# Kernel optimization log

Measured on AMD Instinct MI355X. Metric: run time of the kernel, lower is better.

Reference implementation:

```python
import jax, jax.numpy as jnp
import numpy as np

B, S, DIM = 2, 2048, 2048
NH, NKV = 32, 8
HD = DIM // NH          # 64
NREP = NH // NKV        # 4
BASE = 10000.0


def setup_inputs() -> dict:
    key = jax.random.key(0)
    ks = jax.random.split(key, 5)
    x = jax.random.normal(ks[0], (B, S, DIM), dtype=jnp.float32)
    # causal mask, 1 = keep, 0 = masked (matches masked_fill(mask == 0, -inf))
    mask = jnp.tril(jnp.ones((S, S), dtype=jnp.float32))[None, None]
    scale = 0.02
    Wq = jax.random.normal(ks[1], (DIM, NH * HD), dtype=jnp.float32) * scale
    Wk = jax.random.normal(ks[2], (DIM, NKV * HD), dtype=jnp.float32) * scale
    Wv = jax.random.normal(ks[3], (DIM, NKV * HD), dtype=jnp.float32) * scale
    Wo = jax.random.normal(ks[4], (NH * HD, DIM), dtype=jnp.float32) * scale
    return {"x": x, "mask": mask, "Wq": Wq, "Wk": Wk, "Wv": Wv, "Wo": Wo}


def _rope_cos_sin(seq_len, head_dim, dtype):
    inv_freq = 1.0 / (BASE ** (jnp.arange(0, head_dim, 2, dtype=jnp.float32) / head_dim))
    t = jnp.arange(seq_len, dtype=jnp.float32)
    freqs = t[:, None] * inv_freq[None, :]            # [S, HD/2]
    return jnp.cos(freqs).astype(dtype), jnp.sin(freqs).astype(dtype)


def _apply_rope(x, cos, sin):
    # x: [B, H, S, HD]; cos/sin: [S, HD/2] broadcast over B,H
    x1, x2 = jnp.split(x, 2, axis=-1)
    c = cos[None, None]
    s = sin[None, None]
    return jnp.concatenate([x1 * c - x2 * s, x2 * c + x1 * s], axis=-1)


def reference(x, mask, Wq, Wk, Wv, Wo):
    b, s, _ = x.shape
    q = (x @ Wq).reshape(b, s, NH, HD).transpose(0, 2, 1, 3)   # [B,NH,S,HD]
    k = (x @ Wk).reshape(b, s, NKV, HD).transpose(0, 2, 1, 3)  # [B,NKV,S,HD]
    v = (x @ Wv).reshape(b, s, NKV, HD).transpose(0, 2, 1, 3)
    cos, sin = _rope_cos_sin(s, HD, x.dtype)
    q = _apply_rope(q, cos, sin)
    k = _apply_rope(k, cos, sin)
    # GQA: repeat kv heads
    k = jnp.repeat(k, NREP, axis=1)
    v = jnp.repeat(v, NREP, axis=1)
    scale = HD ** -0.5
    attn = jnp.einsum('bhqd,bhkd->bhqk', q, k) * scale
    attn = jnp.where(mask == 0, -jnp.inf, attn)
    attn = jax.nn.softmax(attn, axis=-1)
    out = jnp.einsum('bhqk,bhkd->bhqd', attn, v)
    out = out.transpose(0, 2, 1, 3).reshape(b, s, NH * HD)
    return out @ Wo
```

## Files before the change

### kernel.cpp

```cpp
#include <hip/hip_runtime.h>
#include <stdint.h>

typedef __attribute__((ext_vector_type(8))) short short8;
typedef __attribute__((ext_vector_type(4))) short short4v;
typedef __attribute__((ext_vector_type(4))) float float4v;
typedef __attribute__((ext_vector_type(16))) float f32x16;
typedef __attribute__((ext_vector_type(4))) int int4v;
typedef __attribute__((ext_vector_type(2))) int int2v;
typedef __attribute__((ext_vector_type(2))) unsigned int uint2v;

#define DEV __device__ __forceinline__

DEV ushort f2bf(float f){
  uint32_t u = __float_as_uint(f);
  u = (u + 0x7fffu + ((u >> 16) & 1u)) >> 16;
  return (ushort)u;
}
DEV float bf2f(ushort h){
  uint32_t u = ((uint32_t)h) << 16;
  return __uint_as_float(u);
}

DEV void gload16(const void* g, void* l){
  __builtin_amdgcn_global_load_lds((const __attribute__((address_space(1))) void*)g,
                                   (__attribute__((address_space(3))) void*)l, 16, 0, 0);
}

DEV uint32_t cvtpk(float lo, float hi){
  uint32_t d;
  asm("v_cvt_pk_bf16_f32 %0, %1, %2" : "=v"(d) : "v"(lo), "v"(hi));
  return d;
}

DEV uint2v plswap2(uint32_t a, uint32_t b){
  return __builtin_amdgcn_permlane32_swap(a, b, false, false);
}

__global__ __launch_bounds__(256) void k_prep(const float* __restrict__ x, const float* __restrict__ Wq,
                                              const float* __restrict__ Wk, const float* __restrict__ Wv,
                                              const float* __restrict__ Wo,
                                              ushort* __restrict__ xb, ushort* __restrict__ wqkvt,
                                              ushort* __restrict__ wot,
                                              float* __restrict__ cost, float* __restrict__ sint,
                                              float qscale){
  __shared__ float tile[32][33];
  const int bid = blockIdx.x;
  if (bid < 10240){
    const float* src; ushort* dst; int N, K, bx, by; float scale;
    if (bid < 4096){ src = Wq; dst = wqkvt; N = 2048; K = 2048; scale = qscale; bx = bid & 63; by = bid >> 6; }
    else if (bid < 5120){ int lb = bid - 4096; src = Wk; dst = wqkvt + (size_t)2048 * 2048; N = 512; K = 2048; scale = 1.f; bx = lb & 15; by = lb >> 4; }
    else if (bid < 6144){ int lb = bid - 5120; src = Wv; dst = wqkvt + (size_t)2560 * 2048; N = 512; K = 2048; scale = 1.f; bx = lb & 15; by = lb >> 4; }
    else { int lb = bid - 6144; src = Wo; dst = wot; N = 2048; K = 2048; scale = 1.f; bx = lb & 63; by = lb >> 6; }
    int c0 = bx * 32, r0 = by * 32;
    int tx = threadIdx.x & 31, ty = threadIdx.x >> 5;
    #pragma unroll
    for (int i = 0; i < 32; i += 8)
      tile[ty + i][tx] = src[(size_t)(r0 + ty + i) * N + (c0 + tx)];
    __syncthreads();
    #pragma unroll
    for (int i = 0; i < 32; i += 8)
      dst[(size_t)(c0 + ty + i) * K + (r0 + tx)] = f2bf(tile[tx][ty + i] * scale);
  } else if (bid < 10496){
    int i = (bid - 10240) * 256 + threadIdx.x;
    int s = i >> 5, d = i & 31;
    float inv = powf(10000.0f, -(float)d / 32.0f);
    float ang = (float)s * inv;
    float sv, cv;
    sincosf(ang, &sv, &cv);
    cost[i] = cv;
    sint[i] = sv;
  } else {
    int i = (bid - 10496) * 256 + threadIdx.x;
    float4v v = *(const float4v*)(x + (size_t)i * 4);
    short4v o;
    o[0] = (short)f2bf(v[0]); o[1] = (short)f2bf(v[1]);
    o[2] = (short)f2bf(v[2]); o[3] = (short)f2bf(v[3]);
    *(short4v*)(xb + (size_t)i * 4) = o;
  }
}

template<int BM, int BN, bool OUTF32, int MINW>
__global__ __launch_bounds__(512, MINW) void k_gemm8(const ushort* __restrict__ A, const ushort* __restrict__ Bt,
                                                     void* __restrict__ Cp, int M, int N, int K, int nbx){
  constexpr int WM = BM / 2, WN = BN / 4;
  constexpr int MR = WM / 16, NR = WN / 16, MP = MR / 4;
  constexpr int AISS = BM / 64, BISS = BN / 64;
  constexpr int BUFB = (BM + BN) * 128;
  __shared__ char lds[2 * BUFB];

  int wg = blockIdx.x;
  int cpx = (int)gridDim.x >> 3;
  wg = (wg & 7) * cpx + (wg >> 3);
  const int bn = wg % nbx, bm = wg / nbx;
  const int tid = threadIdx.x;
  const int w = tid >> 6, l = tid & 63, l15 = l & 15, hi = l >> 4;
  const int wr = w >> 2, wc = w & 3;

  const int r8 = tid >> 3;
  const int ce = ((tid & 7) ^ (r8 & 7)) << 3;
  const ushort* ag = A + (size_t)(bm * BM + r8) * K + ce;
  const ushort* bg = Bt + (size_t)(bn * BN + r8) * K + ce;

  float4v acc[MR][NR];
  #pragma unroll
  for (int a = 0; a < MR; ++a)
    #pragma unroll
    for (int b = 0; b < NR; ++b)
      acc[a][b] = (float4v){0.f, 0.f, 0.f, 0.f};

  auto stage = [&](int kt, int buf){
    char* ab = lds + buf * BUFB;
    char* bb = ab + BM * 128;
    #pragma unroll
    for (int i = 0; i < AISS; ++i)
      gload16(ag + (size_t)(i * 64) * K + kt * 64, ab + i * 8192 + tid * 16);
    #pragma unroll
    for (int i = 0; i < BISS; ++i)
      gload16(bg + (size_t)(i * 64) * K + kt * 64, bb + i * 8192 + tid * 16);
  };
  auto lda = [&](const char* ab, int mf, int kk)->short8{
    int row = wr * WM + mf * 16 + l15;
    int a = (row * 128 + kk * 64 + hi * 16) ^ ((row & 7) << 4);
    return *(const short8*)(ab + a);
  };
  auto ldb = [&](const char* bb, int nf, int kk)->short8{
    int row = wc * WN + nf * 16 + l15;
    int a = (row * 128 + kk * 64 + hi * 16) ^ ((row & 7) << 4);
    return *(const short8*)(bb + a);
  };

  const int nkt = K >> 6;
  stage(0, 0);
  for (int t = 0; t < nkt; ++t){
    asm volatile("s_waitcnt vmcnt(0)" ::: "memory");
    __builtin_amdgcn_s_barrier();
    __builtin_amdgcn_sched_barrier(0);
    if (t + 1 < nkt) stage(t + 1, (t + 1) & 1);

    const char* ab = lds + (t & 1) * BUFB;
    const char* bb = ab + BM * 128;
    short8 bfr[NR][2];
    #pragma unroll
    for (int nf = 0; nf < NR; ++nf){ bfr[nf][0] = ldb(bb, nf, 0); bfr[nf][1] = ldb(bb, nf, 1); }
    short8 af[MP][2];
    #pragma unroll
    for (int ml = 0; ml < MP; ++ml){ af[ml][0] = lda(ab, ml, 0); af[ml][1] = lda(ab, ml, 1); }

    #pragma unroll
    for (int p = 0; p < 4; ++p){
      asm volatile("s_waitcnt lgkmcnt(0)" ::: "memory");
      __builtin_amdgcn_sched_barrier(0);
      __builtin_amdgcn_s_setprio(1);
      #pragma unroll
      for (int ml = 0; ml < MP; ++ml)
        #pragma unroll
        for (int nf = 0; nf < NR; ++nf){
          const int mf = p * MP + ml;
          acc[mf][nf] = __builtin_amdgcn_mfma_f32_16x16x32_bf16(af[ml][0], bfr[nf][0], acc[mf][nf], 0, 0, 0);
          acc[mf][nf] = __builtin_amdgcn_mfma_f32_16x16x32_bf16(af[ml][1], bfr[nf][1], acc[mf][nf], 0, 0, 0);
        }
      __builtin_amdgcn_s_setprio(0);
      __builtin_amdgcn_sched_barrier(0);
      if (p < 3){
        #pragma unroll
        for (int ml = 0; ml < MP; ++ml){
          af[ml][0] = lda(ab, (p + 1) * MP + ml, 0);
          af[ml][1] = lda(ab, (p + 1) * MP + ml, 1);
        }
      }
    }
  }

  #pragma unroll
  for (int mf = 0; mf < MR; ++mf){
    int row0 = bm * BM + wr * WM + mf * 16 + hi * 4;
    #pragma unroll
    for (int nf = 0; nf < NR; ++nf){
      int col = bn * BN + wc * WN + nf * 16 + l15;
      #pragma unroll
      for (int reg = 0; reg < 4; ++reg){
        size_t idx = (size_t)(row0 + reg) * N + col;
        if constexpr (OUTF32) ((float*)Cp)[idx] = acc[mf][nf][reg];
        else                  ((ushort*)Cp)[idx] = f2bf(acc[mf][nf][reg]);
      }
    }
  }
}

__global__ __launch_bounds__(256) void k_rope_vt(ushort* __restrict__ qkv, const float* __restrict__ cost,
                                                 const float* __restrict__ sint, ushort* __restrict__ vt){
  __shared__ ushort tile[64][72];
  const int bid = blockIdx.x;
  if (bid < 5120){
    int t = bid * 256 + threadIdx.x;
    int row = t / 320;
    int rem = t - row * 320;
    int head = rem >> 3, d0 = (rem & 7) * 4;
    int s = row & 2047;
    ushort* p = qkv + (size_t)row * 3072 + head * 64 + d0;
    short4v a = *(short4v*)p;
    short4v b = *(short4v*)(p + 32);
    float4v c  = *(const float4v*)(cost + s * 32 + d0);
    float4v sn = *(const float4v*)(sint + s * 32 + d0);
    short4v na, nb;
    #pragma unroll
    for (int j = 0; j < 4; ++j){
      float x1 = bf2f((ushort)a[j]), x2 = bf2f((ushort)b[j]);
      na[j] = (short)f2bf(x1 * c[j] - x2 * sn[j]);
      nb[j] = (short)f2bf(x2 * c[j] + x1 * sn[j]);
    }
    *(short4v*)p = na;
    *(short4v*)(p + 32) = nb;
  } else {
    int lb = bid - 5120;
    int g = lb >> 5, st = lb & 31;
    int b = g >> 3, hk = g & 7;
    const ushort* src = qkv + (size_t)(b * 2048 + st * 64) * 3072 + 2560 + hk * 64;
    int tid = threadIdx.x;
    #pragma unroll
    for (int i = 0; i < 2; ++i){
      int r = i * 32 + (tid >> 3), c8 = (tid & 7) * 8;
      short8 v = *(const short8*)(src + (size_t)r * 3072 + c8);
      #pragma unroll
      for (int j = 0; j < 8; ++j) tile[r][c8 + j] = (ushort)v[j];
    }
    __syncthreads();
    ushort* dst = vt + (size_t)g * 64 * 2048 + st * 64;
    #pragma unroll
    for (int i = 0; i < 2; ++i){
      int d = i * 32 + (tid >> 3), s8 = (tid & 7) * 8;
      short8 ov;
      #pragma unroll
      for (int j = 0; j < 8; ++j) ov[j] = (short)tile[s8 + j][d];
      *(short8*)(dst + (size_t)d * 2048 + s8) = ov;
    }
  }
}

__global__ __launch_bounds__(256) void k_attn9(const ushort* __restrict__ qkv, const ushort* __restrict__ vt,
                                               ushort* __restrict__ att,
                                               ushort* __restrict__ pO, float* __restrict__ pl){
  __shared__ __align__(16) char lds[2][16384];
  const int id = blockIdx.x;
  int gidx, hloc, qb, t0, t1, slot = 0;
  bool split;
  if (id < 1024){
    int xcd = id & 7, s2 = id >> 3;
    gidx = xcd * 2 + (s2 >> 6);
    int idx6 = s2 & 63;
    hloc = idx6 & 3;
    int c = (idx6 >> 2) & 1;
    qb = 15 - (idx6 >> 3);
    int nt = 2 * qb + 2, hh = nt >> 1;
    t0 = c * hh; t1 = t0 + hh;
    split = true;
    slot = (((gidx * 4 + hloc) * 8) + (15 - qb)) * 2 + c;
  } else {
    int id2 = id - 1024;
    int xcd = id2 & 7, s3 = id2 >> 3;
    gidx = xcd * 2 + (s3 & 1);
    int idx5 = s3 >> 1;
    hloc = idx5 & 3;
    qb = 7 - (idx5 >> 2);
    t0 = 0; t1 = 2 * qb + 2;
    split = false;
  }
  const int b = gidx >> 3, hk = gidx & 7;
  const int h = hk * 4 + hloc;
  const int tid = threadIdx.x;
  const int w = tid >> 6, l = tid & 63, ql = l & 31, g = l >> 5;
  const int qw = qb * 128 + w * 32;
  const int diag_t = (qw + 31) >> 6;
  const int swz = (ql & 7) << 4;

  short8 qf[4];
  {
    const ushort* qbase = qkv + (size_t)(b * 2048 + qw + ql) * 3072 + h * 64 + g * 8;
    #pragma unroll
    for (int ds = 0; ds < 4; ++ds) qf[ds] = *(const short8*)(qbase + ds * 16);
  }
  short8 onesf;
  #pragma unroll
  for (int i = 0; i < 8; ++i) onesf[i] = (short)0x3F80;

  f32x16 o0, o1, ladd;
  #pragma unroll
  for (int r = 0; r < 16; ++r){ o0[r] = 0.f; o1[r] = 0.f; ladd[r] = 0.f; }

  const int srow = tid >> 3;
  const int ce = ((tid & 7) ^ (srow & 7)) << 3;
  const ushort* kg = qkv + (size_t)(b * 2048 + srow) * 3072 + 2048 + hk * 64 + ce;
  const ushort* vg = vt + (size_t)gidx * 64 * 2048 + (size_t)srow * 2048 + ce;

  auto stage = [&](int t, int buf){
    char* lb = lds[buf];
    #pragma unroll
    for (int i = 0; i < 2; ++i)
      gload16(kg + (size_t)(t * 64 + i * 32) * 3072, lb + i * 4096 + tid * 16);
    #pragma unroll
    for (int i = 0; i < 2; ++i)
      gload16(vg + (size_t)(i * 32) * 2048 + t * 64, lb + 8192 + i * 4096 + tid * 16);
  };

  stage(t0, t0 & 1);
  for (int t = t0; t < t1; ++t){
    asm volatile("s_waitcnt vmcnt(0)" ::: "memory");
    __builtin_amdgcn_s_barrier();
    __builtin_amdgcn_sched_barrier(0);
    if (t + 1 < t1) stage(t + 1, (t + 1) & 1);

    if (t <= diag_t){
      const char* Kb = lds[t & 1];
      const char* Vb = Kb + 8192;

      f32x16 sa0, sa1;
      #pragma unroll
      for (int r = 0; r < 16; ++r){ sa0[r] = 0.f; sa1[r] = 0.f; }
      __builtin_amdgcn_s_setprio(1);
      #pragma unroll
      for (int ds = 0; ds < 4; ++ds){
        int cb = (ds * 32 + g * 16) ^ swz;
        short8 k0 = *(const short8*)(Kb + ql * 128 + cb);
        short8 k1 = *(const short8*)(Kb + (32 + ql) * 128 + cb);
        sa0 = __builtin_amdgcn_mfma_f32_32x32x16_bf16(k0, qf[ds], sa0, 0, 0, 0);
        sa1 = __builtin_amdgcn_mfma_f32_32x32x16_bf16(k1, qf[ds], sa1, 0, 0, 0);
      }
      __builtin_amdgcn_s_setprio(0);

      if (t == diag_t){
        int thr = qw + ql - t * 64;
        #pragma unroll
        for (int r = 0; r < 16; ++r){
          int kl = (r & 3) + 8 * (r >> 2) + 4 * g;
          sa0[r] = (kl > thr) ? -3e38f : sa0[r];
          sa1[r] = (kl + 32 > thr) ? -3e38f : sa1[r];
        }
      }

      uint32_t wds[2][8];
      #pragma unroll
      for (int u = 0; u < 8; ++u){
        float a0 = __builtin_amdgcn_exp2f(sa0[2 * u]);
        float a1 = __builtin_amdgcn_exp2f(sa0[2 * u + 1]);
        wds[0][u] = cvtpk(a0, a1);
        float b0 = __builtin_amdgcn_exp2f(sa1[2 * u]);
        float b1 = __builtin_amdgcn_exp2f(sa1[2 * u + 1]);
        wds[1][u] = cvtpk(b0, b1);
      }

      __builtin_amdgcn_s_setprio(1);
      #pragma unroll
      for (int ks = 0; ks < 4; ++ks){
        const int s2 = ks >> 1, c4 = (ks & 1) * 4;
        uint2v e0 = plswap2(wds[s2][c4 + 0], wds[s2][c4 + 2]);
        uint2v e1 = plswap2(wds[s2][c4 + 1], wds[s2][c4 + 3]);
        union { int4v w4; short8 s8; } pb;
        pb.w4[0] = (int)e0[0]; pb.w4[1] = (int)e1[0];
        pb.w4[2] = (int)e0[1]; pb.w4[3] = (int)e1[1];
        int cb = (ks * 32 + g * 16) ^ swz;
        short8 v0 = *(const short8*)(Vb + ql * 128 + cb);
        short8 v1 = *(const short8*)(Vb + (32 + ql) * 128 + cb);
        o0 = __builtin_amdgcn_mfma_f32_32x32x16_bf16(v0, pb.s8, o0, 0, 0, 0);
        o1 = __builtin_amdgcn_mfma_f32_32x32x16_bf16(v1, pb.s8, o1, 0, 0, 0);
        ladd = __builtin_amdgcn_mfma_f32_32x32x16_bf16(onesf, pb.s8, ladd, 0, 0, 0);
      }
      __builtin_amdgcn_s_setprio(0);
    }
  }

  if (split){
    ushort* po = pO + (size_t)slot * 8192 + (size_t)(w * 32 + ql) * 64;
    #pragma unroll
    for (int dm = 0; dm < 2; ++dm){
      #pragma unroll
      for (int rg = 0; rg < 4; ++rg){
        float f0 = dm ? o1[4 * rg + 0] : o0[4 * rg + 0];
        float f1 = dm ? o1[4 * rg + 1] : o0[4 * rg + 1];
        float f2 = dm ? o1[4 * rg + 2] : o0[4 * rg + 2];
        float f3 = dm ? o1[4 * rg + 3] : o0[4 * rg + 3];
        int2v wv;
        wv[0] = (int)cvtpk(f0, f1);
        wv[1] = (int)cvtpk(f2, f3);
        *(int2v*)(po + dm * 32 + 8 * rg + 4 * g) = wv;
      }
    }
    if (!g) pl[slot * 128 + w * 32 + ql] = ladd[0];
  } else {
    float invl = 1.0f / ladd[0];
    ushort* ob = att + (size_t)(b * 2048 + qw + ql) * 2048 + h * 64;
    #pragma unroll
    for (int dm = 0; dm < 2; ++dm){
      #pragma unroll
      for (int rg = 0; rg < 4; ++rg){
        float f0 = (dm ? o1[4 * rg + 0] : o0[4 * rg + 0]) * invl;
        float f1 = (dm ? o1[4 * rg + 1] : o0[4 * rg + 1]) * invl;
        float f2 = (dm ? o1[4 * rg + 2] : o0[4 * rg + 2]) * invl;
        float f3 = (dm ? o1[4 * rg + 3] : o0[4 * rg + 3]) * invl;
        int2v wv;
        wv[0] = (int)cvtpk(f0, f1);
        wv[1] = (int)cvtpk(f2, f3);
        *(int2v*)(ob + dm * 32 + 8 * rg + 4 * g) = wv;
      }
    }
  }
}

__global__ __launch_bounds__(256) void k_combine(const ushort* __restrict__ pO, const float* __restrict__ pl,
                                                 ushort* __restrict__ att){
  const int id = blockIdx.x;
  const int pid = id >> 1, half = id & 1;
  const int head = pid >> 3, qb8 = pid & 7;
  const int qb = 15 - qb8;
  const int gidx = head >> 2, hloc = head & 3;
  const int b = gidx >> 3, hk = gidx & 7;
  const int h = hk * 4 + hloc;
  const int s0 = (head * 8 + qb8) * 2;
  const int tid = threadIdx.x;
  const int r = half * 64 + (tid >> 2);
  const int cc = (tid & 3) * 16;
  const ushort* A = pO + (size_t)s0 * 8192 + (size_t)r * 64 + cc;
  const ushort* B = A + 8192;
  float lsum = pl[s0 * 128 + r] + pl[(s0 + 1) * 128 + r];
  float inv = 1.0f / lsum;
  short8 xa0 = *(const short8*)A, xa1 = *(const short8*)(A + 8);
  short8 xb0 = *(const short8*)B, xb1 = *(const short8*)(B + 8);
  ushort* dst = att + (size_t)(b * 2048 + qb * 128 + r) * 2048 + h * 64 + cc;
  int4v w0, w1;
  #pragma unroll
  for (int j = 0; j < 4; ++j){
    float e0 = (bf2f((ushort)xa0[2 * j]) + bf2f((ushort)xb0[2 * j])) * inv;
    float e1 = (bf2f((ushort)xa0[2 * j + 1]) + bf2f((ushort)xb0[2 * j + 1])) * inv;
    w0[j] = (int)cvtpk(e0, e1);
    float e2 = (bf2f((ushort)xa1[2 * j]) + bf2f((ushort)xb1[2 * j])) * inv;
    float e3 = (bf2f((ushort)xa1[2 * j + 1]) + bf2f((ushort)xb1[2 * j + 1])) * inv;
    w1[j] = (int)cvtpk(e2, e3);
  }
  *(int4v*)dst = w0;
  *(int4v*)(dst + 8) = w1;
}

extern "C" void kernel_launch(void* const* d_in, const int* in_sizes, int n_in,
                              void* d_out, int out_size, void* d_ws, size_t ws_size,
                              hipStream_t stream) {
  const float* x  = (const float*)d_in[0];
  const float* Wq = (const float*)d_in[2];
  const float* Wk = (const float*)d_in[3];
  const float* Wv = (const float*)d_in[4];
  const float* Wo = (const float*)d_in[5];

  char* ws = (char*)d_ws;
  ushort* xb    = (ushort*)(ws);
  ushort* wqkvt = (ushort*)(ws + (16u << 20));
  ushort* wot   = (ushort*)(ws + (28u << 20));
  ushort* qkv   = (ushort*)(ws + (36u << 20));
  ushort* att   = (ushort*)(ws + (60u << 20));
  ushort* vt    = (ushort*)(ws + (76u << 20));
  float*  cost  = (float*)(ws + (80u << 20));
  float*  sint  = (float*)(ws + (80u << 20) + 262144);

  ushort* pO = xb;
  float*  pl = (float*)wqkvt;

  const float qscale = 0.125f * 1.4426950408889634f;

  k_prep<<<18688, 256, 0, stream>>>(x, Wq, Wk, Wv, Wo, xb, wqkvt, wot, cost, sint, qscale);
  k_gemm8<128, 192, false, 4><<<512, 512, 0, stream>>>(xb, wqkvt, qkv, 4096, 3072, 2048, 16);
  k_rope_vt<<<5632, 256, 0, stream>>>(qkv, cost, sint, vt);
  k_attn9<<<1536, 256, 0, stream>>>(qkv, vt, att, pO, pl);
  k_combine<<<1024, 256, 0, stream>>>(pO, pl, att);
  k_gemm8<128, 128, true, 4><<<512, 512, 0, stream>>>(att, wot, d_out, 4096, 2048, 2048, 16);
}
```

Measured before the change: 176.7 us.

## Rebalance causal attention work by pairing short and long query blocks per workgroup

Replaces the previous scheme (long query blocks split in two halves, short blocks one per workgroup) with a table-driven schedule. Each workgroup either processes a pair of complementary query blocks (qb and 7-qb) in sequence, or one half of a long block's key range. This cuts the launch from 1536 to 1280 workgroups with roughly equal work each, which should reduce tail imbalance. It also adds an occupancy hint of 5 in the launch bounds. The combine kernel's slot indexing is updated to match. The trade-offs are serial segments inside one workgroup and a possible register cap from the launch-bounds hint.

```diff
diff --git a/kernel.cpp b/kernel.cpp
--- a/kernel.cpp
+++ b/kernel.cpp
@@ -237,55 +237,29 @@
   }
 }
 
-__global__ __launch_bounds__(256) void k_attn9(const ushort* __restrict__ qkv, const ushort* __restrict__ vt,
-                                               ushort* __restrict__ att,
-                                               ushort* __restrict__ pO, float* __restrict__ pl){
+__global__ __launch_bounds__(256, 5) void k_attn11(const ushort* __restrict__ qkv, const ushort* __restrict__ vt,
+                                                   ushort* __restrict__ att,
+                                                   ushort* __restrict__ pO, float* __restrict__ pl){
+  static const signed char IT_Q[20] = {7,15,8,14, 6,15,8,14, 5,13,9,12, 4,13,9,12, 10,11,10,11};
+  static const signed char IT_H[20] = {-1,0,0,0, -1,1,1,1, -1,0,0,0, -1,1,1,1, 0,0,1,1};
   __shared__ __align__(16) char lds[2][16384];
   const int id = blockIdx.x;
-  int gidx, hloc, qb, t0, t1, slot = 0;
-  bool split;
-  if (id < 1024){
-    int xcd = id & 7, s2 = id >> 3;
-    gidx = xcd * 2 + (s2 >> 6);
-    int idx6 = s2 & 63;
-    hloc = idx6 & 3;
-    int c = (idx6 >> 2) & 1;
-    qb = 15 - (idx6 >> 3);
-    int nt = 2 * qb + 2, hh = nt >> 1;
-    t0 = c * hh; t1 = t0 + hh;
-    split = true;
-    slot = (((gidx * 4 + hloc) * 8) + (15 - qb)) * 2 + c;
-  } else {
-    int id2 = id - 1024;
-    int xcd = id2 & 7, s3 = id2 >> 3;
-    gidx = xcd * 2 + (s3 & 1);
-    int idx5 = s3 >> 1;
-    hloc = idx5 & 3;
-    qb = 7 - (idx5 >> 2);
-    t0 = 0; t1 = 2 * qb + 2;
-    split = false;
-  }
+  const int xcd = id & 7, lid = id >> 3;
+  const int gh = lid / 80, li = lid - gh * 80;
+  const int gidx = xcd * 2 + gh;
   const int b = gidx >> 3, hk = gidx & 7;
+  const int hloc = li / 20, it = li - hloc * 20;
   const int h = hk * 4 + hloc;
+  const int qb0 = IT_Q[it];
+  const int hh = IT_H[it];
+  const int nseg = (hh < 0) ? 2 : 1;
   const int tid = threadIdx.x;
   const int w = tid >> 6, l = tid & 63, ql = l & 31, g = l >> 5;
-  const int qw = qb * 128 + w * 32;
-  const int diag_t = (qw + 31) >> 6;
   const int swz = (ql & 7) << 4;
 
-  short8 qf[4];
-  {
-    const ushort* qbase = qkv + (size_t)(b * 2048 + qw + ql) * 3072 + h * 64 + g * 8;
-    #pragma unroll
-    for (int ds = 0; ds < 4; ++ds) qf[ds] = *(const short8*)(qbase + ds * 16);
-  }
   short8 onesf;
   #pragma unroll
   for (int i = 0; i < 8; ++i) onesf[i] = (short)0x3F80;
-
-  f32x16 o0, o1, ladd;
-  #pragma unroll
-  for (int r = 0; r < 16; ++r){ o0[r] = 0.f; o1[r] = 0.f; ladd[r] = 0.f; }
 
   const int srow = tid >> 3;
   const int ce = ((tid & 7) ^ (srow & 7)) << 3;
@@ -302,104 +276,126 @@
       gload16(vg + (size_t)(i * 32) * 2048 + t * 64, lb + 8192 + i * 4096 + tid * 16);
   };
 
-  stage(t0, t0 & 1);
-  for (int t = t0; t < t1; ++t){
-    asm volatile("s_waitcnt vmcnt(0)" ::: "memory");
-    __builtin_amdgcn_s_barrier();
-    __builtin_amdgcn_sched_barrier(0);
-    if (t + 1 < t1) stage(t + 1, (t + 1) & 1);
-
-    if (t <= diag_t){
-      const char* Kb = lds[t & 1];
-      const char* Vb = Kb + 8192;
-
-      f32x16 sa0, sa1;
-      #pragma unroll
-      for (int r = 0; r < 16; ++r){ sa0[r] = 0.f; sa1[r] = 0.f; }
-      __builtin_amdgcn_s_setprio(1);
-      #pragma unroll
-      for (int ds = 0; ds < 4; ++ds){
-        int cb = (ds * 32 + g * 16) ^ swz;
-        short8 k0 = *(const short8*)(Kb + ql * 128 + cb);
-        short8 k1 = *(const short8*)(Kb + (32 + ql) * 128 + cb);
-        sa0 = __builtin_amdgcn_mfma_f32_32x32x16_bf16(k0, qf[ds], sa0, 0, 0, 0);
-        sa1 = __builtin_amdgcn_mfma_f32_32x32x16_bf16(k1, qf[ds], sa1, 0, 0, 0);
+  for (int seg = 0; seg < nseg; ++seg){
+    const int qb = (hh < 0) ? (seg ? (7 - qb0) : qb0) : qb0;
+    int t0, t1;
+    bool partial;
+    if (hh < 0){ t0 = 0; t1 = 2 * qb + 2; partial = false; }
+    else { t0 = hh ? (qb0 + 1) : 0; t1 = hh ? (2 * qb0 + 2) : (qb0 + 1); partial = true; }
+    const int qw = qb * 128 + w * 32;
+    const int diag_t = (qw + 31) >> 6;
+
+    short8 qf[4];
+    {
+      const ushort* qbase = qkv + (size_t)(b * 2048 + qw + ql) * 3072 + h * 64 + g * 8;
+      #pragma unroll
+      for (int ds = 0; ds < 4; ++ds) qf[ds] = *(const short8*)(qbase + ds * 16);
+    }
+
+    f32x16 o0, o1, ladd;
+    #pragma unroll
+    for (int r = 0; r < 16; ++r){ o0[r] = 0.f; o1[r] = 0.f; ladd[r] = 0.f; }
+
+    stage(t0, t0 & 1);
+    for (int t = t0; t < t1; ++t){
+      asm volatile("s_waitcnt vmcnt(0)" ::: "memory");
+      __builtin_amdgcn_s_barrier();
+      __builtin_amdgcn_sched_barrier(0);
+      if (t + 1 < t1) stage(t + 1, (t + 1) & 1);
+
+      if (t <= diag_t){
+        const char* Kb = lds[t & 1];
+        const char* Vb = Kb + 8192;
+
+        f32x16 sa0, sa1;
+        #pragma unroll
+        for (int r = 0; r < 16; ++r){ sa0[r] = 0.f; sa1[r] = 0.f; }
+        __builtin_amdgcn_s_setprio(1);
+        #pragma unroll
+        for (int ds = 0; ds < 4; ++ds){
+          int cb = (ds * 32 + g * 16) ^ swz;
+          short8 k0 = *(const short8*)(Kb + ql * 128 + cb);
+          short8 k1 = *(const short8*)(Kb + (32 + ql) * 128 + cb);
+          sa0 = __builtin_amdgcn_mfma_f32_32x32x16_bf16(k0, qf[ds], sa0, 0, 0, 0);
+          sa1 = __builtin_amdgcn_mfma_f32_32x32x16_bf16(k1, qf[ds], sa1, 0, 0, 0);
+        }
+        __builtin_amdgcn_s_setprio(0);
+
+        if (t == diag_t){
+          int thr = qw + ql - t * 64;
+          #pragma unroll
+          for (int r = 0; r < 16; ++r){
+            int kl = (r & 3) + 8 * (r >> 2) + 4 * g;
+            sa0[r] = (kl > thr) ? -3e38f : sa0[r];
+            sa1[r] = (kl + 32 > thr) ? -3e38f : sa1[r];
+          }
+        }
+
+        uint32_t wds[2][8];
+        #pragma unroll
+        for (int u = 0; u < 8; ++u){
+          float a0 = __builtin_amdgcn_exp2f(sa0[2 * u]);
+          float a1 = __builtin_amdgcn_exp2f(sa0[2 * u + 1]);
+          wds[0][u] = cvtpk(a0, a1);
+          float b0 = __builtin_amdgcn_exp2f(sa1[2 * u]);
+          float b1 = __builtin_amdgcn_exp2f(sa1[2 * u + 1]);
+          wds[1][u] = cvtpk(b0, b1);
+        }
+
+        __builtin_amdgcn_s_setprio(1);
+        #pragma unroll
+        for (int ks = 0; ks < 4; ++ks){
+          const int s2 = ks >> 1, c4 = (ks & 1) * 4;
+          uint2v e0 = plswap2(wds[s2][c4 + 0], wds[s2][c4 + 2]);
+          uint2v e1 = plswap2(wds[s2][c4 + 1], wds[s2][c4 + 3]);
+          union { int4v w4; short8 s8; } pb;
+          pb.w4[0] = (int)e0[0]; pb.w4[1] = (int)e1[0];
+          pb.w4[2] = (int)e0[1]; pb.w4[3] = (int)e1[1];
+          int cb = (ks * 32 + g * 16) ^ swz;
+          short8 v0 = *(const short8*)(Vb + ql * 128 + cb);
+          short8 v1 = *(const short8*)(Vb + (32 + ql) * 128 + cb);
+          o0 = __builtin_amdgcn_mfma_f32_32x32x16_bf16(v0, pb.s8, o0, 0, 0, 0);
+          o1 = __builtin_amdgcn_mfma_f32_32x32x16_bf16(v1, pb.s8, o1, 0, 0, 0);
+          ladd = __builtin_amdgcn_mfma_f32_32x32x16_bf16(onesf, pb.s8, ladd, 0, 0, 0);
+        }
+        __builtin_amdgcn_s_setprio(0);
       }
-      __builtin_amdgcn_s_setprio(0);
-
-      if (t == diag_t){
-        int thr = qw + ql - t * 64;
-        #pragma unroll
-        for (int r = 0; r < 16; ++r){
-          int kl = (r & 3) + 8 * (r >> 2) + 4 * g;
-          sa0[r] = (kl > thr) ? -3e38f : sa0[r];
-          sa1[r] = (kl + 32 > thr) ? -3e38f : sa1[r];
+    }
+
+    if (partial){
+      const int slot = ((gidx * 4 + hloc) * 8 + (qb0 - 8)) * 2 + hh;
+      ushort* po = pO + (size_t)slot * 8192 + (size_t)(w * 32 + ql) * 64;
+      #pragma unroll
+      for (int dm = 0; dm < 2; ++dm){
+        #pragma unroll
+        for (int rg = 0; rg < 4; ++rg){
+          float f0 = dm ? o1[4 * rg + 0] : o0[4 * rg + 0];
+          float f1 = dm ? o1[4 * rg + 1] : o0[4 * rg + 1];
+          float f2 = dm ? o1[4 * rg + 2] : o0[4 * rg + 2];
+          float f3 = dm ? o1[4 * rg + 3] : o0[4 * rg + 3];
+          int2v wv;
+          wv[0] = (int)cvtpk(f0, f1);
+          wv[1] = (int)cvtpk(f2, f3);
+          *(int2v*)(po + dm * 32 + 8 * rg + 4 * g) = wv;
         }
       }
-
-      uint32_t wds[2][8];
-      #pragma unroll
-      for (int u = 0; u < 8; ++u){
-        float a0 = __builtin_amdgcn_exp2f(sa0[2 * u]);
-        float a1 = __builtin_amdgcn_exp2f(sa0[2 * u + 1]);
-        wds[0][u] = cvtpk(a0, a1);
-        float b0 = __builtin_amdgcn_exp2f(sa1[2 * u]);
-        float b1 = __builtin_amdgcn_exp2f(sa1[2 * u + 1]);
-        wds[1][u] = cvtpk(b0, b1);
-      }
-
-      __builtin_amdgcn_s_setprio(1);
-      #pragma unroll
-      for (int ks = 0; ks < 4; ++ks){
-        const int s2 = ks >> 1, c4 = (ks & 1) * 4;
-        uint2v e0 = plswap2(wds[s2][c4 + 0], wds[s2][c4 + 2]);
-        uint2v e1 = plswap2(wds[s2][c4 + 1], wds[s2][c4 + 3]);
-        union { int4v w4; short8 s8; } pb;
-        pb.w4[0] = (int)e0[0]; pb.w4[1] = (int)e1[0];
-        pb.w4[2] = (int)e0[1]; pb.w4[3] = (int)e1[1];
-        int cb = (ks * 32 + g * 16) ^ swz;
-        short8 v0 = *(const short8*)(Vb + ql * 128 + cb);
-        short8 v1 = *(const short8*)(Vb + (32 + ql) * 128 + cb);
-        o0 = __builtin_amdgcn_mfma_f32_32x32x16_bf16(v0, pb.s8, o0, 0, 0, 0);
-        o1 = __builtin_amdgcn_mfma_f32_32x32x16_bf16(v1, pb.s8, o1, 0, 0, 0);
-        ladd = __builtin_amdgcn_mfma_f32_32x32x16_bf16(onesf, pb.s8, ladd, 0, 0, 0);
-      }
-      __builtin_amdgcn_s_setprio(0);
-    }
-  }
-
-  if (split){
-    ushort* po = pO + (size_t)slot * 8192 + (size_t)(w * 32 + ql) * 64;
-    #pragma unroll
-    for (int dm = 0; dm < 2; ++dm){
-      #pragma unroll
-      for (int rg = 0; rg < 4; ++rg){
-        float f0 = dm ? o1[4 * rg + 0] : o0[4 * rg + 0];
-        float f1 = dm ? o1[4 * rg + 1] : o0[4 * rg + 1];
-        float f2 = dm ? o1[4 * rg + 2] : o0[4 * rg + 2];
-        float f3 = dm ? o1[4 * rg + 3] : o0[4 * rg + 3];
-        int2v wv;
-        wv[0] = (int)cvtpk(f0, f1);
-        wv[1] = (int)cvtpk(f2, f3);
-        *(int2v*)(po + dm * 32 + 8 * rg + 4 * g) = wv;
-      }
-    }
-    if (!g) pl[slot * 128 + w * 32 + ql] = ladd[0];
-  } else {
-    float invl = 1.0f / ladd[0];
-    ushort* ob = att + (size_t)(b * 2048 + qw + ql) * 2048 + h * 64;
-    #pragma unroll
-    for (int dm = 0; dm < 2; ++dm){
-      #pragma unroll
-      for (int rg = 0; rg < 4; ++rg){
-        float f0 = (dm ? o1[4 * rg + 0] : o0[4 * rg + 0]) * invl;
-        float f1 = (dm ? o1[4 * rg + 1] : o0[4 * rg + 1]) * invl;
-        float f2 = (dm ? o1[4 * rg + 2] : o0[4 * rg + 2]) * invl;
-        float f3 = (dm ? o1[4 * rg + 3] : o0[4 * rg + 3]) * invl;
-        int2v wv;
-        wv[0] = (int)cvtpk(f0, f1);
-        wv[1] = (int)cvtpk(f2, f3);
-        *(int2v*)(ob + dm * 32 + 8 * rg + 4 * g) = wv;
+      if (!g) pl[slot * 128 + w * 32 + ql] = ladd[0];
+    } else {
+      float invl = 1.0f / ladd[0];
+      ushort* ob = att + (size_t)(b * 2048 + qw + ql) * 2048 + h * 64;
+      #pragma unroll
+      for (int dm = 0; dm < 2; ++dm){
+        #pragma unroll
+        for (int rg = 0; rg < 4; ++rg){
+          float f0 = (dm ? o1[4 * rg + 0] : o0[4 * rg + 0]) * invl;
+          float f1 = (dm ? o1[4 * rg + 1] : o0[4 * rg + 1]) * invl;
+          float f2 = (dm ? o1[4 * rg + 2] : o0[4 * rg + 2]) * invl;
+          float f3 = (dm ? o1[4 * rg + 3] : o0[4 * rg + 3]) * invl;
+          int2v wv;
+          wv[0] = (int)cvtpk(f0, f1);
+          wv[1] = (int)cvtpk(f2, f3);
+          *(int2v*)(ob + dm * 32 + 8 * rg + 4 * g) = wv;
+        }
       }
     }
   }
@@ -409,12 +405,12 @@
                                                  ushort* __restrict__ att){
   const int id = blockIdx.x;
   const int pid = id >> 1, half = id & 1;
-  const int head = pid >> 3, qb8 = pid & 7;
-  const int qb = 15 - qb8;
+  const int head = pid >> 3, qbi = pid & 7;
+  const int qb = 8 + qbi;
   const int gidx = head >> 2, hloc = head & 3;
   const int b = gidx >> 3, hk = gidx & 7;
   const int h = hk * 4 + hloc;
-  const int s0 = (head * 8 + qb8) * 2;
+  const int s0 = (head * 8 + qbi) * 2;
   const int tid = threadIdx.x;
   const int r = half * 64 + (tid >> 2);
   const int cc = (tid & 3) * 16;
@@ -466,7 +462,7 @@
   k_prep<<<18688, 256, 0, stream>>>(x, Wq, Wk, Wv, Wo, xb, wqkvt, wot, cost, sint, qscale);
   k_gemm8<128, 192, false, 4><<<512, 512, 0, stream>>>(xb, wqkvt, qkv, 4096, 3072, 2048, 16);
   k_rope_vt<<<5632, 256, 0, stream>>>(qkv, cost, sint, vt);
-  k_attn9<<<1536, 256, 0, stream>>>(qkv, vt, att, pO, pl);
+  k_attn11<<<1280, 256, 0, stream>>>(qkv, vt, att, pO, pl);
   k_combine<<<1024, 256, 0, stream>>>(pO, pl, att);
   k_gemm8<128, 128, true, 4><<<512, 512, 0, stream>>>(att, wot, d_out, 4096, 2048, 2048, 16);
 }
```

Measured after the change: 324.5 us. 1.84x slower.
